# Kernel optimization log

Measured on AMD Instinct MI355X. Metric: run time of the kernel, lower is better.

Reference implementation:

```python
import jax, jax.numpy as jnp
import numpy as np

B, C, H, W = 16, 512, 64, 64
K = 32


def setup_inputs() -> dict:
    key = jax.random.key(0)
    k1, k2, k3 = jax.random.split(key, 3)
    std = 1.0 / (64 * C) ** 0.5
    x = jax.random.normal(k1, (B, C, H, W), dtype=jnp.float32)
    codewords = jax.random.uniform(k2, (K, C), dtype=jnp.float32, minval=-std, maxval=std)
    scale = jax.random.uniform(k3, (K,), dtype=jnp.float32, minval=-1.0, maxval=0.0)
    return {"x": x, "codewords": codewords, "scale": scale}


def reference(x, codewords, scale):
    b, c, h, w = x.shape
    # (b, n, c) with n = h*w spatial positions
    xf = x.reshape(b, c, h * w).transpose(0, 2, 1)
    x2 = jnp.sum(xf * xf, axis=-1)                       # (b, n)
    c2 = jnp.sum(codewords * codewords, axis=-1)          # (k,)
    xc = jnp.einsum('bnc,kc->bnk', xf, codewords)         # (b, n, k)
    logits = scale[None, None, :] * (x2[:, :, None] - 2.0 * xc + c2[None, None, :])
    A = jax.nn.softmax(logits, axis=2)                    # (b, n, k)
    # sum_n A[b,n,k] * (x[b,n,c] - codewords[k,c])
    encoded = jnp.einsum('bnk,bnc->bkc', A, xf) - jnp.einsum('bnk,kc->bkc', A, codewords)
    return encoded
```

## Files before the change

kernel.cpp:

```cpp
#include <hip/hip_runtime.h>
#include <hip/hip_bf16.h>
#include <math.h>

#define BB 16
#define CC 512
#define NN 4096
#define KK 32

typedef __attribute__((ext_vector_type(8))) short short8;
typedef __attribute__((ext_vector_type(4))) float float4v;

static __device__ __forceinline__ unsigned short f2bf(float f) {
  unsigned u = __float_as_uint(f);
  u += 0x7FFF + ((u >> 16) & 1);
  return (unsigned short)(u >> 16);
}


__global__ __launch_bounds__(256) void prep_kernel(
    const float* __restrict__ cw, unsigned short* __restrict__ cwP,
    float* __restrict__ c2, float* __restrict__ asum) {
  int gid = blockIdx.x * 256 + threadIdx.x;
  if (gid < BB * KK) asum[gid] = 0.f;
  {
    int k = gid >> 9;
    int cc = gid & 511;
    int cs = cc & ~31;
    int w5 = cc & 31;
    int q = w5 >> 3, j = w5 & 7;
    int src_c = cs + 2 * q + (j & 1) + ((j >> 1) << 3);
    cwP[gid] = f2bf(cw[k * CC + src_c]);
  }
  __shared__ float c2p[KK][8];
  if (blockIdx.x == 0) {
    int k = threadIdx.x >> 3, j = threadIdx.x & 7;
    const float* row = cw + k * CC + j * 64;
    float s = 0.f;
    for (int i = 0; i < 64; ++i) s = fmaf(row[i], row[i], s);
    c2p[k][j] = s;
    __syncthreads();
    if (threadIdx.x < KK) {
      float t = 0.f;
      for (int j2 = 0; j2 < 8; ++j2) t += c2p[threadIdx.x][j2];
      c2[threadIdx.x] = t;
    }
  }
}

#define XP 72
__global__ __launch_bounds__(256, 2) void fused_kernel(
    const float* __restrict__ x, const unsigned short* __restrict__ cwP,
    const float* __restrict__ c2g, const float* __restrict__ scale,
    float* __restrict__ partials, float* __restrict__ asum) {
  const int b = blockIdx.x >> 5;
  const int chunk = blockIdx.x & 31;
  const int t = threadIdx.x;
  const int w = t >> 6;
  const int l = t & 63;
  const int l15 = l & 15;
  const int q = l >> 4;

  __shared__ char smem[512 * XP * 2 + 32 * XP * 2 + 256];
  unsigned short* Xl = (unsigned short*)smem;
  unsigned short* As = (unsigned short*)(smem + 512 * XP * 2);
  float* Sx2p = (float*)(smem + 512 * XP * 2);
  float* Sx2 = (float*)(smem + 512 * XP * 2 + 32 * XP * 2);

  const float* xb0 = x + (size_t)b * CC * NN + chunk * 128;

  const float sc0 = scale[l15], sc1 = scale[16 + l15];
  const float cc0 = c2g[l15], cc1 = c2g[16 + l15];

  float4v acc[8][2];
#pragma unroll
  for (int ct = 0; ct < 8; ++ct)
#pragma unroll
    for (int m = 0; m < 2; ++m) acc[ct][m] = (float4v){0.f, 0.f, 0.f, 0.f};
  float s0acc = 0.f, s1acc = 0.f;

  const int f4 = t & 15;
  const int cr = t >> 4;

  for (int sub = 0; sub < 2; ++sub) {
    const float* xb = xb0 + sub * 64;

    {
      float4v x2p = {0.f, 0.f, 0.f, 0.f};
#pragma unroll 8
      for (int i = 0; i < 32; ++i) {
        const int c = cr + 16 * i;
        float4v v = *(const float4v*)(xb + (size_t)c * NN + 4 * f4);
        x2p.x = fmaf(v.x, v.x, x2p.x);
        x2p.y = fmaf(v.y, v.y, x2p.y);
        x2p.z = fmaf(v.z, v.z, x2p.z);
        x2p.w = fmaf(v.w, v.w, x2p.w);
        unsigned p0 = (unsigned)f2bf(v.x) | ((unsigned)f2bf(v.y) << 16);
        unsigned p1 = (unsigned)f2bf(v.z) | ((unsigned)f2bf(v.w) << 16);
        *(uint2*)&Xl[c * XP + 4 * f4] = make_uint2(p0, p1);
      }
      *(float4v*)&Sx2p[cr * 68 + 4 * f4] = x2p;
    }
    __syncthreads();
    if (t < 64) {
      float s = 0.f;
#pragma unroll
      for (int r = 0; r < 16; ++r) s += Sx2p[r * 68 + t];
      Sx2[t] = s;
    }
    __syncthreads();

    float4v p0 = {0.f, 0.f, 0.f, 0.f};
    float4v p1 = {0.f, 0.f, 0.f, 0.f};
    const int nrow = w * 16 + l15;
    for (int cs = 0; cs < 512; cs += 32) {
      const int cb2 = cs + 2 * q;
      short8 af;
#pragma unroll
      for (int j = 0; j < 8; ++j) {
        const int c = cb2 + (j & 1) + ((j >> 1) << 3);
        af[j] = (short)Xl[c * XP + nrow];
      }
      short8 b0 = *(const short8*)(cwP + (size_t)l15 * CC + cs + q * 8);
      short8 b1 = *(const short8*)(cwP + (size_t)(16 + l15) * CC + cs + q * 8);
      p0 = __builtin_amdgcn_mfma_f32_16x16x32_bf16(af, b0, p0, 0, 0, 0);
      p1 = __builtin_amdgcn_mfma_f32_16x16x32_bf16(af, b1, p1, 0, 0, 0);
    }

    float a0[4], a1[4];
#pragma unroll
    for (int r = 0; r < 4; ++r) {
      const float xx = Sx2[w * 16 + 4 * q + r];
      float l0 = sc0 * (xx - 2.f * p0[r] + cc0);
      float l1 = sc1 * (xx - 2.f * p1[r] + cc1);
      float m = fmaxf(l0, l1);
      m = fmaxf(m, __shfl_xor(m, 1));
      m = fmaxf(m, __shfl_xor(m, 2));
      m = fmaxf(m, __shfl_xor(m, 4));
      m = fmaxf(m, __shfl_xor(m, 8));
      float e0 = __expf(l0 - m), e1 = __expf(l1 - m);
      float s = e0 + e1;
      s += __shfl_xor(s, 1);
      s += __shfl_xor(s, 2);
      s += __shfl_xor(s, 4);
      s += __shfl_xor(s, 8);
      float inv = 1.0f / s;
      a0[r] = e0 * inv;
      a1[r] = e1 * inv;
    }
    s0acc += a0[0] + a0[1] + a0[2] + a0[3];
    s1acc += a1[0] + a1[1] + a1[2] + a1[3];

    {
      unsigned p00 = (unsigned)f2bf(a0[0]) | ((unsigned)f2bf(a0[1]) << 16);
      unsigned p01 = (unsigned)f2bf(a0[2]) | ((unsigned)f2bf(a0[3]) << 16);
      unsigned p10 = (unsigned)f2bf(a1[0]) | ((unsigned)f2bf(a1[1]) << 16);
      unsigned p11 = (unsigned)f2bf(a1[2]) | ((unsigned)f2bf(a1[3]) << 16);
      const int nc = w * 16 + 4 * q;
      *(uint2*)&As[l15 * XP + nc] = make_uint2(p00, p01);
      *(uint2*)&As[(16 + l15) * XP + nc] = make_uint2(p10, p11);
    }
    __syncthreads();

#pragma unroll
    for (int s = 0; s < 2; ++s) {
      const int nb = s * 32 + q * 8;
      short8 am0 = *(const short8*)&As[l15 * XP + nb];
      short8 am1 = *(const short8*)&As[(16 + l15) * XP + nb];
#pragma unroll
      for (int ct = 0; ct < 8; ++ct) {
        const int c = w * 128 + ct * 16 + l15;
        short8 bx = *(const short8*)&Xl[c * XP + nb];
        acc[ct][0] = __builtin_amdgcn_mfma_f32_16x16x32_bf16(am0, bx, acc[ct][0], 0, 0, 0);
        acc[ct][1] = __builtin_amdgcn_mfma_f32_16x16x32_bf16(am1, bx, acc[ct][1], 0, 0, 0);
      }
    }
    __syncthreads();
  }

  float* pout = partials + (size_t)blockIdx.x * KK * CC;
#pragma unroll
  for (int ct = 0; ct < 8; ++ct) {
    const int c = w * 128 + ct * 16 + l15;
#pragma unroll
    for (int m = 0; m < 2; ++m)
#pragma unroll
      for (int r = 0; r < 4; ++r) {
        int k = 16 * m + 4 * q + r;
        pout[k * CC + c] = acc[ct][m][r];
      }
  }
  s0acc += __shfl_xor(s0acc, 16);
  s0acc += __shfl_xor(s0acc, 32);
  s1acc += __shfl_xor(s1acc, 16);
  s1acc += __shfl_xor(s1acc, 32);
  if (q == 0) {
    atomicAdd(&asum[b * KK + l15], s0acc);
    atomicAdd(&asum[b * KK + 16 + l15], s1acc);
  }
}

__global__ __launch_bounds__(256) void reduce_kernel(
    const float* __restrict__ partials, const float* __restrict__ asum,
    const float* __restrict__ cw, float* __restrict__ out) {
  int idx = blockIdx.x * 256 + threadIdx.x;
  int b = idx >> 12;
  int k = (idx >> 7) & 31;
  int c4 = idx & 127;

  float4v o = {0.f, 0.f, 0.f, 0.f};
  const float4v* pb = (const float4v*)partials + ((size_t)(b * 32) * KK + k) * 128 + c4;
#pragma unroll 8
  for (int p = 0; p < 32; ++p) {
    float4v v = pb[(size_t)p * KK * 128];
    o.x += v.x;
    o.y += v.y;
    o.z += v.z;
    o.w += v.w;
  }
  float4v wv = ((const float4v*)cw)[k * 128 + c4];
  float a = asum[b * KK + k];
  o.x -= a * wv.x;
  o.y -= a * wv.y;
  o.z -= a * wv.z;
  o.w -= a * wv.w;
  ((float4v*)out)[idx] = o;
}

extern "C" void kernel_launch(void* const* d_in, const int* in_sizes, int n_in,
                              void* d_out, int out_size, void* d_ws, size_t ws_size,
                              hipStream_t stream) {
  const float* x = (const float*)d_in[0];
  const float* cw = (const float*)d_in[1];
  const float* scale = (const float*)d_in[2];
  float* out = (float*)d_out;
  char* ws = (char*)d_ws;

  float* c2 = (float*)ws;
  unsigned short* cwP = (unsigned short*)(ws + 128);
  float* asum = (float*)(ws + 32896);
  float* partials = (float*)(ws + 35072);

  prep_kernel<<<64, 256, 0, stream>>>(cw, cwP, c2, asum);
  fused_kernel<<<512, 256, 0, stream>>>(x, cwP, c2, scale, partials, asum);
  reduce_kernel<<<256, 256, 0, stream>>>(partials, asum, cw, out);
}
```

Baseline: 228.8 us.

## Halve per-step spatial tile to 32 positions, raise occupancy to 4 blocks per CU

The kernel now processes 32 spatial positions per sub-step (four steps) instead of 64, which roughly halves the LDS footprint so launch bounds can request 4 blocks per CU. Only two of the four waves compute the logits GEMM and softmax, with roles alternating by block parity, while a third wave reduces x^2. The x^2 partial sums now use cross-lane shuffles instead of an LDS staging pass. The trade-off is more barriers per position, idle waves during the logits phase, and a tighter register budget that could cause spills.

```diff
diff --git a/kernel.cpp b/kernel.cpp
--- a/kernel.cpp
+++ b/kernel.cpp
@@ -8,12 +8,20 @@
 #define KK 32
 
 typedef __attribute__((ext_vector_type(8))) short short8;
+typedef __attribute__((ext_vector_type(4))) short short4v;
 typedef __attribute__((ext_vector_type(4))) float float4v;
 
 static __device__ __forceinline__ unsigned short f2bf(float f) {
   unsigned u = __float_as_uint(f);
   u += 0x7FFF + ((u >> 16) & 1);
   return (unsigned short)(u >> 16);
+}
+
+static __device__ __forceinline__ short8 cat8(short4v a, short4v b) {
+  short8 r;
+  r[0] = a[0]; r[1] = a[1]; r[2] = a[2]; r[3] = a[3];
+  r[4] = b[0]; r[5] = b[1]; r[6] = b[2]; r[7] = b[3];
+  return r;
 }
 
 
@@ -47,8 +55,8 @@
   }
 }
 
-#define XP 72
-__global__ __launch_bounds__(256, 2) void fused_kernel(
+#define XP2 36
+__global__ __launch_bounds__(256, 4) void fused_kernel(
     const float* __restrict__ x, const unsigned short* __restrict__ cwP,
     const float* __restrict__ c2g, const float* __restrict__ scale,
     float* __restrict__ partials, float* __restrict__ asum) {
@@ -59,12 +67,12 @@
   const int l = t & 63;
   const int l15 = l & 15;
   const int q = l >> 4;
-
-  __shared__ char smem[512 * XP * 2 + 32 * XP * 2 + 256];
-  unsigned short* Xl = (unsigned short*)smem;
-  unsigned short* As = (unsigned short*)(smem + 512 * XP * 2);
-  float* Sx2p = (float*)(smem + 512 * XP * 2);
-  float* Sx2 = (float*)(smem + 512 * XP * 2 + 32 * XP * 2);
+  const int wrole = (w + ((blockIdx.x & 1) << 1)) & 3;
+
+  __shared__ unsigned short Xl[CC * XP2];
+  __shared__ unsigned short As[KK * XP2];
+  __shared__ float Sx2w[4 * 32];
+  __shared__ float Sx2[32];
 
   const float* xb0 = x + (size_t)b * CC * NN + chunk * 128;
 
@@ -78,98 +86,102 @@
     for (int m = 0; m < 2; ++m) acc[ct][m] = (float4v){0.f, 0.f, 0.f, 0.f};
   float s0acc = 0.f, s1acc = 0.f;
 
-  const int f4 = t & 15;
-  const int cr = t >> 4;
-
-  for (int sub = 0; sub < 2; ++sub) {
-    const float* xb = xb0 + sub * 64;
-
-    {
-      float4v x2p = {0.f, 0.f, 0.f, 0.f};
+  const int f4 = t & 7;
+  const int cr = t >> 3;
+
+  for (int sub = 0; sub < 4; ++sub) {
+    const float* xb = xb0 + sub * 32;
+
+    float4v x2p = (float4v){0.f, 0.f, 0.f, 0.f};
 #pragma unroll 8
-      for (int i = 0; i < 32; ++i) {
-        const int c = cr + 16 * i;
-        float4v v = *(const float4v*)(xb + (size_t)c * NN + 4 * f4);
-        x2p.x = fmaf(v.x, v.x, x2p.x);
-        x2p.y = fmaf(v.y, v.y, x2p.y);
-        x2p.z = fmaf(v.z, v.z, x2p.z);
-        x2p.w = fmaf(v.w, v.w, x2p.w);
-        unsigned p0 = (unsigned)f2bf(v.x) | ((unsigned)f2bf(v.y) << 16);
-        unsigned p1 = (unsigned)f2bf(v.z) | ((unsigned)f2bf(v.w) << 16);
-        *(uint2*)&Xl[c * XP + 4 * f4] = make_uint2(p0, p1);
-      }
-      *(float4v*)&Sx2p[cr * 68 + 4 * f4] = x2p;
-    }
-    __syncthreads();
-    if (t < 64) {
-      float s = 0.f;
-#pragma unroll
-      for (int r = 0; r < 16; ++r) s += Sx2p[r * 68 + t];
-      Sx2[t] = s;
-    }
-    __syncthreads();
-
-    float4v p0 = {0.f, 0.f, 0.f, 0.f};
-    float4v p1 = {0.f, 0.f, 0.f, 0.f};
-    const int nrow = w * 16 + l15;
-    for (int cs = 0; cs < 512; cs += 32) {
-      const int cb2 = cs + 2 * q;
-      short8 af;
-#pragma unroll
-      for (int j = 0; j < 8; ++j) {
-        const int c = cb2 + (j & 1) + ((j >> 1) << 3);
-        af[j] = (short)Xl[c * XP + nrow];
-      }
-      short8 b0 = *(const short8*)(cwP + (size_t)l15 * CC + cs + q * 8);
-      short8 b1 = *(const short8*)(cwP + (size_t)(16 + l15) * CC + cs + q * 8);
-      p0 = __builtin_amdgcn_mfma_f32_16x16x32_bf16(af, b0, p0, 0, 0, 0);
-      p1 = __builtin_amdgcn_mfma_f32_16x16x32_bf16(af, b1, p1, 0, 0, 0);
-    }
-
-    float a0[4], a1[4];
-#pragma unroll
-    for (int r = 0; r < 4; ++r) {
-      const float xx = Sx2[w * 16 + 4 * q + r];
-      float l0 = sc0 * (xx - 2.f * p0[r] + cc0);
-      float l1 = sc1 * (xx - 2.f * p1[r] + cc1);
-      float m = fmaxf(l0, l1);
-      m = fmaxf(m, __shfl_xor(m, 1));
-      m = fmaxf(m, __shfl_xor(m, 2));
-      m = fmaxf(m, __shfl_xor(m, 4));
-      m = fmaxf(m, __shfl_xor(m, 8));
-      float e0 = __expf(l0 - m), e1 = __expf(l1 - m);
-      float s = e0 + e1;
-      s += __shfl_xor(s, 1);
-      s += __shfl_xor(s, 2);
-      s += __shfl_xor(s, 4);
-      s += __shfl_xor(s, 8);
-      float inv = 1.0f / s;
-      a0[r] = e0 * inv;
-      a1[r] = e1 * inv;
-    }
-    s0acc += a0[0] + a0[1] + a0[2] + a0[3];
-    s1acc += a1[0] + a1[1] + a1[2] + a1[3];
-
-    {
+    for (int i = 0; i < 16; ++i) {
+      const int c = cr + 32 * i;
+      float4v v = *(const float4v*)(xb + (size_t)c * NN + 4 * f4);
+      x2p.x = fmaf(v.x, v.x, x2p.x);
+      x2p.y = fmaf(v.y, v.y, x2p.y);
+      x2p.z = fmaf(v.z, v.z, x2p.z);
+      x2p.w = fmaf(v.w, v.w, x2p.w);
+      unsigned p0 = (unsigned)f2bf(v.x) | ((unsigned)f2bf(v.y) << 16);
+      unsigned p1 = (unsigned)f2bf(v.z) | ((unsigned)f2bf(v.w) << 16);
+      *(uint2*)&Xl[c * XP2 + 4 * f4] = make_uint2(p0, p1);
+    }
+#pragma unroll
+    for (int m = 8; m <= 32; m <<= 1) {
+      x2p.x += __shfl_xor(x2p.x, m);
+      x2p.y += __shfl_xor(x2p.y, m);
+      x2p.z += __shfl_xor(x2p.z, m);
+      x2p.w += __shfl_xor(x2p.w, m);
+    }
+    if (l < 8) *(float4v*)&Sx2w[w * 32 + 4 * l] = x2p;
+    __syncthreads();
+
+    float4v p0 = (float4v){0.f, 0.f, 0.f, 0.f};
+    float4v p1 = (float4v){0.f, 0.f, 0.f, 0.f};
+    if (wrole < 2) {
+      const int nrow = wrole * 16 + l15;
+      for (int cs = 0; cs < 512; cs += 32) {
+        const int cb2 = cs + 2 * q;
+        short8 af;
+#pragma unroll
+        for (int j = 0; j < 8; ++j) {
+          const int c = cb2 + (j & 1) + ((j >> 1) << 3);
+          af[j] = (short)Xl[c * XP2 + nrow];
+        }
+        short8 b0 = *(const short8*)(cwP + (size_t)l15 * CC + cs + q * 8);
+        short8 b1 = *(const short8*)(cwP + (size_t)(16 + l15) * CC + cs + q * 8);
+        p0 = __builtin_amdgcn_mfma_f32_16x16x32_bf16(af, b0, p0, 0, 0, 0);
+        p1 = __builtin_amdgcn_mfma_f32_16x16x32_bf16(af, b1, p1, 0, 0, 0);
+      }
+    } else if (wrole == 2 && l < 32) {
+      Sx2[l] = Sx2w[l] + Sx2w[32 + l] + Sx2w[64 + l] + Sx2w[96 + l];
+    }
+    __syncthreads();
+
+    if (wrole < 2) {
+      float a0[4], a1[4];
+#pragma unroll
+      for (int r = 0; r < 4; ++r) {
+        const float xx = Sx2[wrole * 16 + 4 * q + r];
+        float l0 = sc0 * (xx - 2.f * p0[r] + cc0);
+        float l1 = sc1 * (xx - 2.f * p1[r] + cc1);
+        float m = fmaxf(l0, l1);
+        m = fmaxf(m, __shfl_xor(m, 1));
+        m = fmaxf(m, __shfl_xor(m, 2));
+        m = fmaxf(m, __shfl_xor(m, 4));
+        m = fmaxf(m, __shfl_xor(m, 8));
+        float e0 = __expf(l0 - m), e1 = __expf(l1 - m);
+        float s = e0 + e1;
+        s += __shfl_xor(s, 1);
+        s += __shfl_xor(s, 2);
+        s += __shfl_xor(s, 4);
+        s += __shfl_xor(s, 8);
+        float inv = 1.0f / s;
+        a0[r] = e0 * inv;
+        a1[r] = e1 * inv;
+      }
+      s0acc += a0[0] + a0[1] + a0[2] + a0[3];
+      s1acc += a1[0] + a1[1] + a1[2] + a1[3];
       unsigned p00 = (unsigned)f2bf(a0[0]) | ((unsigned)f2bf(a0[1]) << 16);
       unsigned p01 = (unsigned)f2bf(a0[2]) | ((unsigned)f2bf(a0[3]) << 16);
       unsigned p10 = (unsigned)f2bf(a1[0]) | ((unsigned)f2bf(a1[1]) << 16);
       unsigned p11 = (unsigned)f2bf(a1[2]) | ((unsigned)f2bf(a1[3]) << 16);
-      const int nc = w * 16 + 4 * q;
-      *(uint2*)&As[l15 * XP + nc] = make_uint2(p00, p01);
-      *(uint2*)&As[(16 + l15) * XP + nc] = make_uint2(p10, p11);
-    }
-    __syncthreads();
-
-#pragma unroll
-    for (int s = 0; s < 2; ++s) {
-      const int nb = s * 32 + q * 8;
-      short8 am0 = *(const short8*)&As[l15 * XP + nb];
-      short8 am1 = *(const short8*)&As[(16 + l15) * XP + nb];
+      const int nc = wrole * 16 + 4 * q;
+      *(uint2*)&As[l15 * XP2 + nc] = make_uint2(p00, p01);
+      *(uint2*)&As[(16 + l15) * XP2 + nc] = make_uint2(p10, p11);
+    }
+    __syncthreads();
+
+    {
+      const int nb = q * 8;
+      const short4v* Ap0 = (const short4v*)&As[l15 * XP2 + nb];
+      const short4v* Ap1 = (const short4v*)&As[(16 + l15) * XP2 + nb];
+      short8 am0 = cat8(Ap0[0], Ap0[1]);
+      short8 am1 = cat8(Ap1[0], Ap1[1]);
 #pragma unroll
       for (int ct = 0; ct < 8; ++ct) {
         const int c = w * 128 + ct * 16 + l15;
-        short8 bx = *(const short8*)&Xl[c * XP + nb];
+        const short4v* Bp = (const short4v*)&Xl[c * XP2 + nb];
+        short8 bx = cat8(Bp[0], Bp[1]);
         acc[ct][0] = __builtin_amdgcn_mfma_f32_16x16x32_bf16(am0, bx, acc[ct][0], 0, 0, 0);
         acc[ct][1] = __builtin_amdgcn_mfma_f32_16x16x32_bf16(am1, bx, acc[ct][1], 0, 0, 0);
       }
@@ -193,7 +205,7 @@
   s0acc += __shfl_xor(s0acc, 32);
   s1acc += __shfl_xor(s1acc, 16);
   s1acc += __shfl_xor(s1acc, 32);
-  if (q == 0) {
+  if (wrole < 2 && q == 0) {
     atomicAdd(&asum[b * KK + l15], s0acc);
     atomicAdd(&asum[b * KK + 16 + l15], s1acc);
   }
```

New measurement: 231.6 us. No clear change (+1.2%).
